# Kernel optimization log

Hardware: AMD Instinct MI355X
Metric: run time of the kernel (lower is better)

The kernel has to match this reference:

```python
import jax, jax.numpy as jnp
import numpy as np

B, H, W = 8, 64, 64
DIM_RGB, DIM_PL, EMBED, OUT = 256, 256, 128, 256
BN_EPS = 1e-5


def conv1x1(x, w, b=None):
    # x: (B,C,H,W), w: (D,C) -> (B,D,H,W)
    y = jnp.einsum('bchw,dc->bdhw', x, w)
    if b is not None:
        y = y + b[None, :, None, None]
    return y


def spatial_attention(q, k, v, scale):
    # q,k,v: (B,D,H,W)
    b, d, h, w = q.shape
    n = h * w
    qf = q.reshape(b, d, n).transpose(0, 2, 1)   # (B,N,D)
    kf = k.reshape(b, d, n)                       # (B,D,N)
    vf = v.reshape(b, d, n).transpose(0, 2, 1)   # (B,N,D)
    attn = jax.nn.softmax(jnp.einsum('bnd,bdm->bnm', qf, kf) * scale, axis=-1)
    out = jnp.einsum('bnm,bmd->bnd', attn, vf)   # (B,N,D)
    return out.transpose(0, 2, 1).reshape(b, d, h, w)


def setup_inputs() -> dict:
    key = jax.random.key(0)
    ks = jax.random.split(key, 20)
    s = 0.05
    inp = {
        'f_rgb': jax.random.normal(ks[0], (B, DIM_RGB, H, W), jnp.float32),
        'f_pl': jax.random.normal(ks[1], (B, DIM_PL, H, W), jnp.float32),
        'w_q_rgb': jax.random.normal(ks[2], (EMBED, DIM_RGB), jnp.float32) * s,
        'b_q_rgb': jax.random.normal(ks[3], (EMBED,), jnp.float32) * s,
        'w_k_pl': jax.random.normal(ks[4], (EMBED, DIM_PL), jnp.float32) * s,
        'b_k_pl': jax.random.normal(ks[5], (EMBED,), jnp.float32) * s,
        'w_v_pl': jax.random.normal(ks[6], (EMBED, DIM_PL), jnp.float32) * s,
        'b_v_pl': jax.random.normal(ks[7], (EMBED,), jnp.float32) * s,
        'w_q_pl': jax.random.normal(ks[8], (EMBED, DIM_PL), jnp.float32) * s,
        'b_q_pl': jax.random.normal(ks[9], (EMBED,), jnp.float32) * s,
        'w_k_rgb': jax.random.normal(ks[10], (EMBED, DIM_RGB), jnp.float32) * s,
        'b_k_rgb': jax.random.normal(ks[11], (EMBED,), jnp.float32) * s,
        'w_v_rgb': jax.random.normal(ks[12], (EMBED, DIM_RGB), jnp.float32) * s,
        'b_v_rgb': jax.random.normal(ks[13], (EMBED,), jnp.float32) * s,
        'w_proj': jax.random.normal(ks[14], (OUT, 2 * EMBED), jnp.float32) * s,
        'bn_gamma': jnp.ones((OUT,), jnp.float32),
        'bn_beta': jnp.zeros((OUT,), jnp.float32),
        'bn_mean': jax.random.normal(ks[15], (OUT,), jnp.float32) * 0.01,
        'bn_var': jax.random.uniform(ks[16], (OUT,), jnp.float32, 0.5, 1.5),
    }
    return inp


def reference(f_rgb, f_pl, w_q_rgb, b_q_rgb, w_k_pl, b_k_pl, w_v_pl, b_v_pl,
              w_q_pl, b_q_pl, w_k_rgb, b_k_rgb, w_v_rgb, b_v_rgb,
              w_proj, bn_gamma, bn_beta, bn_mean, bn_var):
    scale = EMBED ** -0.5
    out_rgb2pl = spatial_attention(
        conv1x1(f_rgb, w_q_rgb, b_q_rgb),
        conv1x1(f_pl, w_k_pl, b_k_pl),
        conv1x1(f_pl, w_v_pl, b_v_pl), scale)
    out_pl2rgb = spatial_attention(
        conv1x1(f_pl, w_q_pl, b_q_pl),
        conv1x1(f_rgb, w_k_rgb, b_k_rgb),
        conv1x1(f_rgb, w_v_rgb, b_v_rgb), scale)
    combined = jnp.concatenate([out_rgb2pl, out_pl2rgb], axis=1)  # (B,2E,H,W)
    y = conv1x1(combined, w_proj)  # no bias
    # BatchNorm2d (inference form) + ReLU
    inv = bn_gamma * jax.lax.rsqrt(bn_var + BN_EPS)
    y = y * inv[None, :, None, None] + (bn_beta - bn_mean * inv)[None, :, None, None]
    return jax.nn.relu(y)
```

## Files before the change

### kernel.cpp

```cpp
#include <hip/hip_runtime.h>
#include <hip/hip_bf16.h>
#include <hip/hip_fp16.h>

typedef _Float16 f16;
typedef _Float16 f16x8 __attribute__((ext_vector_type(8)));
typedef _Float16 f16x4 __attribute__((ext_vector_type(4)));
typedef __fp16 hf16x2 __attribute__((ext_vector_type(2)));
typedef float f32x4 __attribute__((ext_vector_type(4)));
typedef float f32x16 __attribute__((ext_vector_type(16)));

#define NP   4096
#define NB   8
#define CINC 256
#define EMB  128
#define OUTC 256
#define BN_EPS 1e-5f

#define DSZ  ((size_t)NB * NP * EMB)
#define TSZ  (2 * DSZ)

__device__ __forceinline__ void gload_lds16(const f16* g, f16* l) {
    __builtin_amdgcn_global_load_lds(
        (const __attribute__((address_space(1))) unsigned int*)g,
        (__attribute__((address_space(3))) unsigned int*)l, 16, 0, 0);
}

__global__ __launch_bounds__(256) void proj_all_kernel(
    const float* __restrict__ Xrgb, const float* __restrict__ Xpl,
    const float* __restrict__ w0, const float* __restrict__ b0,
    const float* __restrict__ w1, const float* __restrict__ b1,
    const float* __restrict__ w2, const float* __restrict__ b2,
    const float* __restrict__ w3, const float* __restrict__ b3,
    const float* __restrict__ w4, const float* __restrict__ b4,
    const float* __restrict__ w5, const float* __restrict__ b5,
    f16* __restrict__ Qt, f16* __restrict__ Kt, f16* __restrict__ Vn)
{
    const int m0 = blockIdx.x * 128;
    const int p  = blockIdx.y;
    const int b  = blockIdx.z;
    const int s  = (p >= 3) ? 1 : 0;
    const int j  = p - s * 3;
    const int tid = threadIdx.x;
    const int w = tid >> 6, lane = tid & 63, quad = lane >> 4, lr = lane & 15;

    const float* X  = s ? Xpl : Xrgb;
    const float* W  = p == 0 ? w0 : p == 1 ? w1 : p == 2 ? w2
                    : p == 3 ? w3 : p == 4 ? w4 : w5;
    const float* Bi = p == 0 ? b0 : p == 1 ? b1 : p == 2 ? b2
                    : p == 3 ? b3 : p == 4 ? b4 : b5;

    __shared__ __align__(16) f16 smem[128 * 72 * 2];
    f16* Al = smem;
    f16* Bl = smem + 128 * 72;

    f32x4 acc[2][8];
    #pragma unroll
    for (int mi = 0; mi < 2; ++mi)
        #pragma unroll
        for (int ni = 0; ni < 8; ++ni) acc[mi][ni] = (f32x4){0.f, 0.f, 0.f, 0.f};

    for (int kt = 0; kt < 4; ++kt) {
        const int kc0 = kt * 64;
        __syncthreads();
        for (int s2 = tid; s2 < 1024; s2 += 256) {
            const int n = s2 & 127, cg = s2 >> 7;
            f16 tmp[8];
            #pragma unroll
            for (int jj = 0; jj < 8; ++jj)
                tmp[jj] = (f16)X[((size_t)b * CINC + kc0 + cg * 8 + jj) * NP + m0 + n];
            *(f16x8*)&Al[n * 72 + cg * 8] = *(const f16x8*)tmp;
        }
        for (int s2 = tid; s2 < 1024; s2 += 256) {
            const int d = s2 >> 3, cg = s2 & 7;
            f16 tmp[8];
            #pragma unroll
            for (int jj = 0; jj < 8; ++jj)
                tmp[jj] = (f16)W[(size_t)d * CINC + kc0 + cg * 8 + jj];
            *(f16x8*)&Bl[d * 72 + cg * 8] = *(const f16x8*)tmp;
        }
        __syncthreads();
        #pragma unroll
        for (int ks = 0; ks < 2; ++ks) {
            f16x8 af[2], bfr[8];
            #pragma unroll
            for (int mi = 0; mi < 2; ++mi)
                af[mi] = *(const f16x8*)&Al[(w * 32 + mi * 16 + lr) * 72 + ks * 32 + quad * 8];
            #pragma unroll
            for (int ni = 0; ni < 8; ++ni)
                bfr[ni] = *(const f16x8*)&Bl[(ni * 16 + lr) * 72 + ks * 32 + quad * 8];
            #pragma unroll
            for (int mi = 0; mi < 2; ++mi)
                #pragma unroll
                for (int ni = 0; ni < 8; ++ni)
                    acc[mi][ni] = __builtin_amdgcn_mfma_f32_16x16x32_f16(
                        af[mi], bfr[ni], acc[mi][ni], 0, 0, 0);
        }
    }

    float bias[8];
    #pragma unroll
    for (int ni = 0; ni < 8; ++ni) bias[ni] = Bi[ni * 16 + lr];

    if (j < 2) {
        f16* out = (j == 0) ? (Qt + (size_t)s * DSZ) : (Kt + (size_t)(1 - s) * DSZ);
        #pragma unroll
        for (int mi = 0; mi < 2; ++mi)
            #pragma unroll
            for (int ni = 0; ni < 8; ++ni)
                #pragma unroll
                for (int r = 0; r < 4; ++r) {
                    const int n = m0 + w * 32 + mi * 16 + quad * 4 + r;
                    out[((size_t)b * NP + n) * EMB + ni * 16 + lr] =
                        (f16)(acc[mi][ni][r] + bias[ni]);
                }
    } else {
        f16* outV = Vn + (size_t)(1 - s) * DSZ;
        __syncthreads();
        f16* T = smem;
        const int quad_p = ((quad & 1) << 1) | (quad >> 1);
        #pragma unroll
        for (int mi = 0; mi < 2; ++mi)
            #pragma unroll
            for (int ni = 0; ni < 8; ++ni)
                #pragma unroll
                for (int r = 0; r < 4; ++r)
                    T[(ni * 16 + lr) * 136 + w * 32 + mi * 16 + quad_p * 4 + r] =
                        (f16)(acc[mi][ni][r] + bias[ni]);
        __syncthreads();
        for (int s2 = tid; s2 < 2048; s2 += 256) {
            const int d = s2 >> 4, n8 = (s2 & 15) * 8;
            *(f16x8*)&outV[((size_t)b * EMB + d) * NP + m0 + n8] =
                *(const f16x8*)&T[d * 136 + n8];
        }
    }
}

__global__ __launch_bounds__(256) __attribute__((amdgpu_waves_per_eu(2, 2)))
void attn_kernel(
    const f16* __restrict__ Qt, const f16* __restrict__ Kt,
    const f16* __restrict__ Vn, f16* __restrict__ combT)
{
    const int bid = blockIdx.x;
    const int g = bid & 15, dir = g >> 3, b = g & 7;
    const int n0 = (bid >> 4) * 128;
    const int tid = threadIdx.x;
    const int w = tid >> 6, lane = tid & 63;
    const int l31 = lane & 31, hi = lane >> 5;
    const int qsub = w >> 1;
    const int kh   = w & 1;

    const f16* __restrict__ Q = Qt + ((size_t)dir * NB + b) * NP * EMB;
    const f16* __restrict__ K = Kt + ((size_t)dir * NB + b) * NP * EMB;
    const f16* __restrict__ V = Vn + ((size_t)dir * NB + b) * (size_t)EMB * NP;

    __shared__ __align__(16) f16 Kl[2][2][32 * 128];
    __shared__ __align__(16) f16 Vl[2][2][128 * 32];

    const int qbase = n0 + qsub * 64;
    const int m00 = kh * 2048;

    f16x8 qf[2][8];
    #pragma unroll
    for (int q32 = 0; q32 < 2; ++q32)
        #pragma unroll
        for (int d16 = 0; d16 < 8; ++d16) {
            f16x8 q = *(const f16x8*)&Q[(size_t)(qbase + q32 * 32 + l31) * EMB + d16 * 16 + hi * 8];
            #pragma unroll
            for (int jj = 0; jj < 8; ++jj)
                q[jj] = q[jj] * (f16)0.12752749f;
            qf[q32][d16] = q;
        }

    f32x16 O[4][2];
    #pragma unroll
    for (int d32 = 0; d32 < 4; ++d32)
        #pragma unroll
        for (int q32 = 0; q32 < 2; ++q32) O[d32][q32] = (f32x16)(0.0f);
    float rs[2] = {0.f, 0.f};

    const int krp = lane >> 4, kp  = lane & 15;
    const int vr4 = lane >> 2, vp4 = lane & 3;

    auto stage_loadK = [&](int t, int buf) {
        const int mk = m00 + t * 32;
        #pragma unroll
        for (int i = 0; i < 4; ++i) {
            const int r = qsub * 16 + i * 4 + krp;
            const int c = kp ^ (r & 7);
            gload_lds16(&K[(size_t)(mk + r) * EMB + c * 8],
                        &Kl[kh][buf][(qsub * 16 + i * 4) * 128]);
        }
    };
    auto stage_loadV = [&](int t, int buf) {
        const int mk = m00 + t * 32;
        #pragma unroll
        for (int i = 0; i < 4; ++i) {
            const int rd = qsub * 64 + i * 16 + vr4;
            const int c = vp4 ^ ((rd >> 1) & 3);
            gload_lds16(&V[(size_t)rd * NP + mk + c * 8],
                        &Vl[kh][buf][(qsub * 64 + i * 16) * 32]);
        }
    };

    stage_loadK(0, 0);
    stage_loadV(0, 0);
    int cur = 0;

    for (int t = 0; t < 64; ++t) {
        __syncthreads();
        if (t < 63) { stage_loadK(t + 1, cur ^ 1); stage_loadV(t + 1, cur ^ 1); }

        const f16* Kb = &Kl[kh][cur][0];
        const f16* Vb = &Vl[kh][cur][0];

        f32x16 s0 = (f32x16)(0.0f), s1 = (f32x16)(0.0f);
        __builtin_amdgcn_s_setprio(1);
        #pragma unroll
        for (int d16 = 0; d16 < 8; ++d16) {
            const int c = (d16 * 2 + hi) ^ (l31 & 7);
            const f16x8 kf = *(const f16x8*)&Kb[l31 * 128 + c * 8];
            s0 = __builtin_amdgcn_mfma_f32_32x32x16_f16(kf, qf[0][d16], s0, 0, 0, 0);
            s1 = __builtin_amdgcn_mfma_f32_32x32x16_f16(kf, qf[1][d16], s1, 0, 0, 0);
        }
        __builtin_amdgcn_s_setprio(0);

        f16x8 pb[2][2];
        #pragma unroll
        for (int q32 = 0; q32 < 2; ++q32) {
            const f32x16 s = q32 ? s1 : s0;
            float sum = 0.f;
            #pragma unroll
            for (int g2 = 0; g2 < 2; ++g2) {
                union { hf16x2 h[4]; f16x8 v; } pu;
                #pragma unroll
                for (int t2 = 0; t2 < 4; ++t2) {
                    const float e0 = __builtin_amdgcn_exp2f(s[g2 * 8 + t2 * 2]);
                    const float e1 = __builtin_amdgcn_exp2f(s[g2 * 8 + t2 * 2 + 1]);
                    sum += e0 + e1;
                    pu.h[t2] = __builtin_amdgcn_cvt_pkrtz(e0, e1);
                }
                pb[g2][q32] = pu.v;
            }
            rs[q32] += sum;
        }

        __builtin_amdgcn_s_setprio(1);
        #pragma unroll
        for (int g2 = 0; g2 < 2; ++g2) {
            #pragma unroll
            for (int d32 = 0; d32 < 4; ++d32) {
                const int row = d32 * 32 + l31;
                const int c = (g2 * 2 + hi) ^ ((l31 >> 1) & 3);
                const f16x8 vf = *(const f16x8*)&Vb[row * 32 + c * 8];
                O[d32][0] = __builtin_amdgcn_mfma_f32_32x32x16_f16(vf, pb[g2][0], O[d32][0], 0, 0, 0);
                O[d32][1] = __builtin_amdgcn_mfma_f32_32x32x16_f16(vf, pb[g2][1], O[d32][1], 0, 0, 0);
            }
        }
        __builtin_amdgcn_s_setprio(0);

        cur ^= 1;
    }

    rs[0] += __shfl_xor(rs[0], 32);
    rs[1] += __shfl_xor(rs[1], 32);

    __syncthreads();
    f16*   Xch = (f16*)&Kl[0][0][0];
    float* rsX = (float*)&Vl[0][0][0];

    if (kh == 1) {
        #pragma unroll
        for (int q32 = 0; q32 < 2; ++q32) {
            const float inv = 1.0f / rs[q32];
            const int ql = qsub * 64 + q32 * 32 + l31;
            #pragma unroll
            for (int d32 = 0; d32 < 4; ++d32)
                #pragma unroll
                for (int tq = 0; tq < 4; ++tq) {
                    f16 o4[4];
                    #pragma unroll
                    for (int jj = 0; jj < 4; ++jj)
                        o4[jj] = (f16)(O[d32][q32][tq * 4 + jj] * inv);
                    *(f16x4*)&Xch[ql * 128 + d32 * 32 + tq * 8 + hi * 4] = *(const f16x4*)o4;
                }
            if (hi == 0) rsX[ql] = rs[q32];
        }
    }
    __syncthreads();
    if (kh == 0) {
        #pragma unroll
        for (int q32 = 0; q32 < 2; ++q32) {
            const int ql = qsub * 64 + q32 * 32 + l31;
            const float rs1 = rsX[ql];
            const float wt = 1.0f / (rs[q32] + rs1);
            const float w1 = rs1 * wt;
            const int n = qbase + q32 * 32 + l31;
            #pragma unroll
            for (int d32 = 0; d32 < 4; ++d32)
                #pragma unroll
                for (int tq = 0; tq < 4; ++tq) {
                    const f16x4 oh = *(const f16x4*)&Xch[ql * 128 + d32 * 32 + tq * 8 + hi * 4];
                    f16 o4[4];
                    #pragma unroll
                    for (int jj = 0; jj < 4; ++jj)
                        o4[jj] = (f16)(O[d32][q32][tq * 4 + jj] * wt + (float)oh[jj] * w1);
                    *(f16x4*)&combT[((size_t)b * NP + n) * OUTC + dir * EMB + d32 * 32 + tq * 8 + hi * 4] =
                        *(const f16x4*)o4;
                }
        }
    }
}

__global__ __launch_bounds__(256) void proj_out_kernel(
    const f16* __restrict__ combT, const float* __restrict__ Wp,
    const float* __restrict__ G, const float* __restrict__ Be,
    const float* __restrict__ Mu, const float* __restrict__ Va,
    float* __restrict__ out)
{
    const int m0 = blockIdx.x * 128;
    const int o0 = blockIdx.y * 128;
    const int b  = blockIdx.z;
    const int tid = threadIdx.x;
    const int w = tid >> 6, lane = tid & 63, quad = lane >> 4, lr = lane & 15;

    __shared__ __align__(16) f16 smem[128 * 72 * 2];
    f16* Al = smem;
    f16* Bl = smem + 128 * 72;

    f32x4 acc[2][8];
    #pragma unroll
    for (int mi = 0; mi < 2; ++mi)
        #pragma unroll
        for (int ni = 0; ni < 8; ++ni) acc[mi][ni] = (f32x4){0.f, 0.f, 0.f, 0.f};

    for (int kt = 0; kt < 4; ++kt) {
        const int kc0 = kt * 64;
        __syncthreads();
        #pragma unroll
        for (int i = 0; i < 4; ++i) {
            const int s2 = i * 256 + tid;
            const int n = s2 >> 3, cg = s2 & 7;
            *(f16x8*)&Al[n * 72 + cg * 8] =
                *(const f16x8*)&combT[((size_t)b * NP + m0 + n) * OUTC + kc0 + cg * 8];
        }
        for (int s2 = tid; s2 < 1024; s2 += 256) {
            const int d = s2 >> 3, cg = s2 & 7;
            f16 tmp[8];
            #pragma unroll
            for (int jj = 0; jj < 8; ++jj)
                tmp[jj] = (f16)Wp[(size_t)(o0 + d) * OUTC + kc0 + cg * 8 + jj];
            *(f16x8*)&Bl[d * 72 + cg * 8] = *(const f16x8*)tmp;
        }
        __syncthreads();
        #pragma unroll
        for (int ks = 0; ks < 2; ++ks) {
            f16x8 af[2], bfr[8];
            #pragma unroll
            for (int mi = 0; mi < 2; ++mi)
                af[mi] = *(const f16x8*)&Al[(w * 32 + mi * 16 + lr) * 72 + ks * 32 + quad * 8];
            #pragma unroll
            for (int ni = 0; ni < 8; ++ni)
                bfr[ni] = *(const f16x8*)&Bl[(ni * 16 + lr) * 72 + ks * 32 + quad * 8];
            #pragma unroll
            for (int mi = 0; mi < 2; ++mi)
                #pragma unroll
                for (int ni = 0; ni < 8; ++ni)
                    acc[mi][ni] = __builtin_amdgcn_mfma_f32_16x16x32_f16(
                        af[mi], bfr[ni], acc[mi][ni], 0, 0, 0);
        }
    }

    __syncthreads();
    f16* T = smem;
    #pragma unroll
    for (int ni = 0; ni < 8; ++ni) {
        const int o = o0 + ni * 16 + lr;
        const float iv = G[o] * rsqrtf(Va[o] + BN_EPS);
        const float sh = Be[o] - Mu[o] * iv;
        #pragma unroll
        for (int mi = 0; mi < 2; ++mi)
            #pragma unroll
            for (int r = 0; r < 4; ++r)
                T[(ni * 16 + lr) * 136 + w * 32 + mi * 16 + quad * 4 + r] =
                    (f16)fmaxf(acc[mi][ni][r] * iv + sh, 0.f);
    }
    __syncthreads();
    for (int s2 = tid; s2 < 2048; s2 += 256) {
        const int o = s2 >> 4, n8 = (s2 & 15) * 8;
        const f16x8 v = *(const f16x8*)&T[o * 136 + n8];
        const size_t off = ((size_t)b * OUTC + o0 + o) * NP + m0 + n8;
        #pragma unroll
        for (int k = 0; k < 8; ++k) out[off + k] = (float)v[k];
    }
}

extern "C" void kernel_launch(void* const* d_in, const int* in_sizes, int n_in,
                              void* d_out, int out_size, void* d_ws, size_t ws_size,
                              hipStream_t stream) {
    const float* f_rgb   = (const float*)d_in[0];
    const float* f_pl    = (const float*)d_in[1];
    const float* w_q_rgb = (const float*)d_in[2];  const float* b_q_rgb = (const float*)d_in[3];
    const float* w_k_pl  = (const float*)d_in[4];  const float* b_k_pl  = (const float*)d_in[5];
    const float* w_v_pl  = (const float*)d_in[6];  const float* b_v_pl  = (const float*)d_in[7];
    const float* w_q_pl  = (const float*)d_in[8];  const float* b_q_pl  = (const float*)d_in[9];
    const float* w_k_rgb = (const float*)d_in[10]; const float* b_k_rgb = (const float*)d_in[11];
    const float* w_v_rgb = (const float*)d_in[12]; const float* b_v_rgb = (const float*)d_in[13];
    const float* w_proj  = (const float*)d_in[14];
    const float* bn_g    = (const float*)d_in[15]; const float* bn_b = (const float*)d_in[16];
    const float* bn_m    = (const float*)d_in[17]; const float* bn_v = (const float*)d_in[18];

    f16* Qt    = (f16*)d_ws;
    f16* Kt    = Qt + TSZ;
    f16* Vn    = Kt + TSZ;
    f16* combT = Vn + TSZ;

    proj_all_kernel<<<dim3(32, 6, 8), 256, 0, stream>>>(
        f_rgb, f_pl,
        w_q_rgb, b_q_rgb, w_k_rgb, b_k_rgb, w_v_rgb, b_v_rgb,
        w_q_pl,  b_q_pl,  w_k_pl,  b_k_pl,  w_v_pl,  b_v_pl,
        Qt, Kt, Vn);

    attn_kernel<<<512, 256, 0, stream>>>(Qt, Kt, Vn, combT);

    proj_out_kernel<<<dim3(32, 2, 8), 256, 0, stream>>>(
        combT, w_proj, bn_g, bn_b, bn_m, bn_v, (float*)d_out);
}
```

Baseline: 394.7 us.

## Give each wave private K/V LDS buffers and drop per-iteration block barriers

The attention kernel now gives each wave its own single K and V tile in LDS and loads it itself, synchronising with explicit vmcnt/lgkmcnt waits instead of a __syncthreads per key tile. The next K tile is issued right after QK^T and the next V tile after PV, so loads overlap with softmax and the other matmul. This removes block-wide barriers, but each wave now loads its own copy of K/V, so two waves share redundant global traffic per tile. The Q scale is also folded into the projection kernel's output, which drops the per-element multiply in the attention prologue.

```diff
diff --git a/kernel.cpp b/kernel.cpp
--- a/kernel.cpp
+++ b/kernel.cpp
@@ -15,6 +15,7 @@
 #define EMB  128
 #define OUTC 256
 #define BN_EPS 1e-5f
+#define QSCALE 0.12752749f
 
 #define DSZ  ((size_t)NB * NP * EMB)
 #define TSZ  (2 * DSZ)
@@ -103,6 +104,7 @@
 
     if (j < 2) {
         f16* out = (j == 0) ? (Qt + (size_t)s * DSZ) : (Kt + (size_t)(1 - s) * DSZ);
+        const float sc = (j == 0) ? QSCALE : 1.0f;
         #pragma unroll
         for (int mi = 0; mi < 2; ++mi)
             #pragma unroll
@@ -111,7 +113,7 @@
                 for (int r = 0; r < 4; ++r) {
                     const int n = m0 + w * 32 + mi * 16 + quad * 4 + r;
                     out[((size_t)b * NP + n) * EMB + ni * 16 + lr] =
-                        (f16)(acc[mi][ni][r] + bias[ni]);
+                        (f16)((acc[mi][ni][r] + bias[ni]) * sc);
                 }
     } else {
         f16* outV = Vn + (size_t)(1 - s) * DSZ;
@@ -153,8 +155,11 @@
     const f16* __restrict__ K = Kt + ((size_t)dir * NB + b) * NP * EMB;
     const f16* __restrict__ V = Vn + ((size_t)dir * NB + b) * (size_t)EMB * NP;
 
-    __shared__ __align__(16) f16 Kl[2][2][32 * 128];
-    __shared__ __align__(16) f16 Vl[2][2][128 * 32];
+    __shared__ __align__(16) f16 Kl[4][32 * 128];
+    __shared__ __align__(16) f16 Vl[4][128 * 32];
+
+    f16* __restrict__ Kbuf = &Kl[w][0];
+    f16* __restrict__ Vbuf = &Vl[w][0];
 
     const int qbase = n0 + qsub * 64;
     const int m00 = kh * 2048;
@@ -163,13 +168,8 @@
     #pragma unroll
     for (int q32 = 0; q32 < 2; ++q32)
         #pragma unroll
-        for (int d16 = 0; d16 < 8; ++d16) {
-            f16x8 q = *(const f16x8*)&Q[(size_t)(qbase + q32 * 32 + l31) * EMB + d16 * 16 + hi * 8];
-            #pragma unroll
-            for (int jj = 0; jj < 8; ++jj)
-                q[jj] = q[jj] * (f16)0.12752749f;
-            qf[q32][d16] = q;
-        }
+        for (int d16 = 0; d16 < 8; ++d16)
+            qf[q32][d16] = *(const f16x8*)&Q[(size_t)(qbase + q32 * 32 + l31) * EMB + d16 * 16 + hi * 8];
 
     f32x16 O[4][2];
     #pragma unroll
@@ -181,56 +181,52 @@
     const int krp = lane >> 4, kp  = lane & 15;
     const int vr4 = lane >> 2, vp4 = lane & 3;
 
-    auto stage_loadK = [&](int t, int buf) {
+    auto stage_loadK = [&](int t) {
         const int mk = m00 + t * 32;
         #pragma unroll
-        for (int i = 0; i < 4; ++i) {
-            const int r = qsub * 16 + i * 4 + krp;
+        for (int i = 0; i < 8; ++i) {
+            const int r = i * 4 + krp;
             const int c = kp ^ (r & 7);
-            gload_lds16(&K[(size_t)(mk + r) * EMB + c * 8],
-                        &Kl[kh][buf][(qsub * 16 + i * 4) * 128]);
+            gload_lds16(&K[(size_t)(mk + r) * EMB + c * 8], Kbuf + (i * 4) * 128);
         }
     };
-    auto stage_loadV = [&](int t, int buf) {
+    auto stage_loadV = [&](int t) {
         const int mk = m00 + t * 32;
         #pragma unroll
-        for (int i = 0; i < 4; ++i) {
-            const int rd = qsub * 64 + i * 16 + vr4;
+        for (int i = 0; i < 8; ++i) {
+            const int rd = i * 16 + vr4;
             const int c = vp4 ^ ((rd >> 1) & 3);
-            gload_lds16(&V[(size_t)rd * NP + mk + c * 8],
-                        &Vl[kh][buf][(qsub * 64 + i * 16) * 32]);
+            gload_lds16(&V[(size_t)rd * NP + mk + c * 8], Vbuf + (i * 16) * 32);
         }
     };
 
-    stage_loadK(0, 0);
-    stage_loadV(0, 0);
-    int cur = 0;
+    stage_loadK(0);
+    stage_loadV(0);
 
     for (int t = 0; t < 64; ++t) {
-        __syncthreads();
-        if (t < 63) { stage_loadK(t + 1, cur ^ 1); stage_loadV(t + 1, cur ^ 1); }
-
-        const f16* Kb = &Kl[kh][cur][0];
-        const f16* Vb = &Vl[kh][cur][0];
+        asm volatile("s_waitcnt vmcnt(8)" ::: "memory");
 
         f32x16 s0 = (f32x16)(0.0f), s1 = (f32x16)(0.0f);
         __builtin_amdgcn_s_setprio(1);
         #pragma unroll
         for (int d16 = 0; d16 < 8; ++d16) {
             const int c = (d16 * 2 + hi) ^ (l31 & 7);
-            const f16x8 kf = *(const f16x8*)&Kb[l31 * 128 + c * 8];
+            const f16x8 kf = *(const f16x8*)&Kbuf[l31 * 128 + c * 8];
             s0 = __builtin_amdgcn_mfma_f32_32x32x16_f16(kf, qf[0][d16], s0, 0, 0, 0);
             s1 = __builtin_amdgcn_mfma_f32_32x32x16_f16(kf, qf[1][d16], s1, 0, 0, 0);
         }
         __builtin_amdgcn_s_setprio(0);
 
-        f16x8 pb[2][2];
-        #pragma unroll
-        for (int q32 = 0; q32 < 2; ++q32) {
-            const f32x16 s = q32 ? s1 : s0;
-            float sum = 0.f;
-            #pragma unroll
-            for (int g2 = 0; g2 < 2; ++g2) {
+        asm volatile("s_waitcnt lgkmcnt(0)" ::: "memory");
+        if (t < 63) stage_loadK(t + 1);
+
+        #pragma unroll
+        for (int g2 = 0; g2 < 2; ++g2) {
+            f16x8 pbq[2];
+            #pragma unroll
+            for (int q32 = 0; q32 < 2; ++q32) {
+                const f32x16 s = q32 ? s1 : s0;
+                float sum = 0.f;
                 union { hf16x2 h[4]; f16x8 v; } pu;
                 #pragma unroll
                 for (int t2 = 0; t2 < 4; ++t2) {
@@ -239,34 +235,35 @@
                     sum += e0 + e1;
                     pu.h[t2] = __builtin_amdgcn_cvt_pkrtz(e0, e1);
                 }
-                pb[g2][q32] = pu.v;
+                pbq[q32] = pu.v;
+                rs[q32] += sum;
             }
-            rs[q32] += sum;
-        }
-
-        __builtin_amdgcn_s_setprio(1);
-        #pragma unroll
-        for (int g2 = 0; g2 < 2; ++g2) {
+            if (g2 == 0) {
+                if (t < 63) asm volatile("s_waitcnt vmcnt(8)" ::: "memory");
+                else        asm volatile("s_waitcnt vmcnt(0)" ::: "memory");
+            }
+            __builtin_amdgcn_s_setprio(1);
             #pragma unroll
             for (int d32 = 0; d32 < 4; ++d32) {
                 const int row = d32 * 32 + l31;
                 const int c = (g2 * 2 + hi) ^ ((l31 >> 1) & 3);
-                const f16x8 vf = *(const f16x8*)&Vb[row * 32 + c * 8];
-                O[d32][0] = __builtin_amdgcn_mfma_f32_32x32x16_f16(vf, pb[g2][0], O[d32][0], 0, 0, 0);
-                O[d32][1] = __builtin_amdgcn_mfma_f32_32x32x16_f16(vf, pb[g2][1], O[d32][1], 0, 0, 0);
+                const f16x8 vf = *(const f16x8*)&Vbuf[row * 32 + c * 8];
+                O[d32][0] = __builtin_amdgcn_mfma_f32_32x32x16_f16(vf, pbq[0], O[d32][0], 0, 0, 0);
+                O[d32][1] = __builtin_amdgcn_mfma_f32_32x32x16_f16(vf, pbq[1], O[d32][1], 0, 0, 0);
             }
-        }
-        __builtin_amdgcn_s_setprio(0);
-
-        cur ^= 1;
+            __builtin_amdgcn_s_setprio(0);
+        }
+
+        asm volatile("s_waitcnt lgkmcnt(0)" ::: "memory");
+        if (t < 63) stage_loadV(t + 1);
     }
 
     rs[0] += __shfl_xor(rs[0], 32);
     rs[1] += __shfl_xor(rs[1], 32);
 
     __syncthreads();
-    f16*   Xch = (f16*)&Kl[0][0][0];
-    float* rsX = (float*)&Vl[0][0][0];
+    f16*   Xch = (f16*)&Kl[0][0];
+    float* rsX = (float*)&Vl[0][0];
 
     if (kh == 1) {
         #pragma unroll
```

New measurement: 397.3 us. Within noise of the previous version (+0.7%).
